# Kernel optimization log

Measured on AMD Instinct MI355X. Metric: run time of the kernel, lower is better.

Reference implementation:

```python
import jax, jax.numpy as jnp
import numpy as np
import math

EMBED_DIM = 256
NUM_HEADS = 8
FFN_DIM = 1024
EPS = 1e-5


def layer_norm(x, g, b):
    mu = jnp.mean(x, axis=-1, keepdims=True)
    var = jnp.var(x, axis=-1, keepdims=True)
    return (x - mu) / jnp.sqrt(var + EPS) * g + b


def setup_inputs() -> dict:
    key = jax.random.key(0)
    ks = jax.random.split(key, 10)
    B, L, D, F = 4, 2048, EMBED_DIM, FFN_DIM
    x = jax.random.normal(ks[0], (B, L, D), dtype=jnp.float32)
    mask = jnp.ones((B, L), dtype=jnp.int32)
    # FFN params (PyTorch Linear default-ish scale)
    W1 = jax.random.normal(ks[1], (D, F), dtype=jnp.float32) / np.sqrt(D)
    b1 = jnp.zeros((F,), dtype=jnp.float32)
    W2 = jax.random.normal(ks[2], (F, D), dtype=jnp.float32) / np.sqrt(F)
    b2 = jnp.zeros((D,), dtype=jnp.float32)
    g1 = jnp.ones((D,), dtype=jnp.float32)
    be1 = jnp.zeros((D,), dtype=jnp.float32)
    g2 = jnp.ones((D,), dtype=jnp.float32)
    be2 = jnp.zeros((D,), dtype=jnp.float32)
    return {"x": x, "mask": mask, "W1": W1, "b1": b1, "W2": W2, "b2": b2,
            "g1": g1, "be1": be1, "g2": g2, "be2": be2}


def quantum_attention(x, mask):
    B, L, D = x.shape
    H, dk = NUM_HEADS, D // NUM_HEADS
    xh = x.reshape(B, L, H, dk).transpose(0, 2, 1, 3)  # [B,H,L,dk]
    # per-token mean over batch and heads -> [L, dk]
    m = jnp.mean(xh, axis=(0, 1))
    # closed form of the single-qubit RX circuit: P(|1>) = sin^2(angle/2)
    dot = m @ m.T  # [L, L]
    ang = jnp.clip(dot, -math.pi, math.pi)
    scores = jnp.sin(ang * 0.5) ** 2  # [L, L], shared across B and H
    attn = jnp.broadcast_to(scores[None, None], (B, H, L, L))
    attn = jnp.where(mask[:, None, None, :] == 0, -1e9, attn)
    attn = jax.nn.softmax(attn, axis=-1)
    out = jnp.einsum('bhij,bhjd->bhid', attn, xh)  # values are xh itself
    return out.transpose(0, 2, 1, 3).reshape(B, L, D)


def reference(x, mask, W1, b1, W2, b2, g1, be1, g2, be2):
    attn_out = quantum_attention(x, mask)
    h = layer_norm(x + attn_out, g1, be1)
    ffn = jax.nn.relu(h @ W1 + b1) @ W2 + b2
    return layer_norm(h + ffn, g2, be2)
```

## Files before the change

kernel.cpp:

```cpp
#include <hip/hip_runtime.h>
#include <hip/hip_bf16.h>


#define B_ 4
#define L_ 2048
#define D_ 256
#define F_ 1024
#define PI_F 3.14159265358979323846f

typedef __bf16 bf16x8 __attribute__((ext_vector_type(8)));
typedef float floatx4 __attribute__((ext_vector_type(4)));
typedef unsigned short ushortx4 __attribute__((ext_vector_type(4)));
typedef unsigned short ushortx8 __attribute__((ext_vector_type(8)));

#define WAIT_VM(n) asm volatile("s_waitcnt vmcnt(" #n ")" ::: "memory")
#define WAIT_LGKM() asm volatile("s_waitcnt lgkmcnt(0)" ::: "memory")
#define SCHED0() __builtin_amdgcn_sched_barrier(0)
#define BARRIER() do { SCHED0(); __builtin_amdgcn_s_barrier(); SCHED0(); } while (0)

__device__ __forceinline__ unsigned short f2bf(float f) {
    unsigned int u = __float_as_uint(f);
    u = (u + 0x7FFFu + ((u >> 16) & 1u)) >> 16;
    return (unsigned short)u;
}
__device__ __forceinline__ float bf2f(unsigned short u) {
    union { unsigned int i; float f; } v; v.i = ((unsigned int)u) << 16; return v.f;
}

__device__ __forceinline__ void async_cp16(unsigned short* lds, const unsigned short* g) {
    __builtin_amdgcn_global_load_lds(
        (const __attribute__((address_space(1))) unsigned int*)g,
        (__attribute__((address_space(3))) unsigned int*)lds, 16, 0, 0);
}

__global__ __launch_bounds__(256) void k_prep(const float* __restrict__ x,
                                              const float* __restrict__ W1,
                                              const float* __restrict__ W2,
                                              const int* __restrict__ mask,
                                              unsigned short* __restrict__ mb,
                                              unsigned short* __restrict__ XmT,
                                              unsigned short* __restrict__ W1T,
                                              unsigned short* __restrict__ W2T) {
    __shared__ float tile[32][33];
    int r = blockIdx.x, t = threadIdx.x;
    if (r >= 2560) {
        if (r < 2816) {
            int idx = (r - 2560) * 256 + t;
            int l = idx >> 5, k = idx & 31;
            float s = 0.f;
#pragma unroll
            for (int b = 0; b < B_; b++) {
                const float* xp = x + ((size_t)(b * L_ + l)) * D_ + k;
#pragma unroll
                for (int h = 0; h < 8; h++) s += xp[h * 32];
            }
            mb[idx] = f2bf(s * (1.f / 32.f));
        } else {
#pragma unroll
            for (int c = 0; c < 32; c++) {
                int e = c * 256 + t;
                int b = e >> 11, j = e & (L_ - 1);
                XmT[(size_t)(1024 + b) * L_ + j] = mask[b * L_ + j] ? 0x3F80 : 0;
            }
        }
        return;
    }
    const float* in; unsigned short* outp; int R, C; const int* mrow = nullptr; size_t bo = 0;
    int bx, by;
    if (r < 2048) {
        int z = r >> 9, rem = r & 511; by = rem >> 3; bx = rem & 7;
        in = x; outp = XmT; R = L_; C = 256; bo = (size_t)z * R * C; mrow = mask + z * L_;
    } else if (r < 2304) {
        int rem = r - 2048; bx = rem & 31; by = rem >> 5;
        in = W1; outp = W1T; R = 256; C = 1024;
    } else {
        int rem = r - 2304; bx = rem & 7; by = rem >> 3;
        in = W2; outp = W2T; R = 1024; C = 256;
    }
    int r0 = by * 32, c0 = bx * 32;
    int tx = t & 31, ty = t >> 5;
#pragma unroll
    for (int rr = 0; rr < 4; rr++) {
        int rw = ty + rr * 8;
        tile[rw][tx] = in[bo + (size_t)(r0 + rw) * C + c0 + tx];
    }
    float mfac = 1.f;
    if (mrow) mfac = mrow[r0 + tx] ? 1.f : 0.f;
    __syncthreads();
#pragma unroll
    for (int rr = 0; rr < 4; rr++) {
        int c = ty + rr * 8;
        outp[bo + (size_t)(c0 + c) * R + r0 + tx] = f2bf(tile[tx][c] * mfac);
    }
}

__global__ __launch_bounds__(256) void k_scores_mfma(const unsigned short* __restrict__ mb,
                                                     unsigned short* __restrict__ E) {
    const int t = threadIdx.x, lane = t & 63, wid = t >> 6;
    const int wm = (wid >> 1) * 64, wn = (wid & 1) * 32;
    const int lr = lane & 15, lq = lane >> 4;
    int m0 = blockIdx.y * 128, n0 = blockIdx.x * 64;
    bf16x8 af[4], bfr[2];
#pragma unroll
    for (int i = 0; i < 4; i++)
        af[i] = *(const bf16x8*)(mb + (size_t)(m0 + wm + i * 16 + lr) * 32 + lq * 8);
#pragma unroll
    for (int j = 0; j < 2; j++)
        bfr[j] = *(const bf16x8*)(mb + (size_t)(n0 + wn + j * 16 + lr) * 32 + lq * 8);
    floatx4 acc[4][2];
#pragma unroll
    for (int i = 0; i < 4; i++)
#pragma unroll
        for (int j = 0; j < 2; j++) {
            acc[i][j] = (floatx4){0.f, 0.f, 0.f, 0.f};
            acc[i][j] = __builtin_amdgcn_mfma_f32_16x16x32_bf16(af[i], bfr[j], acc[i][j], 0, 0, 0);
        }
#pragma unroll
    for (int i = 0; i < 4; i++)
#pragma unroll
        for (int j = 0; j < 2; j++)
#pragma unroll
            for (int r = 0; r < 4; r++) {
                int row = m0 + wm + i * 16 + lq * 4 + r;
                int col = n0 + wn + j * 16 + lr;
                float d = fminf(fmaxf(acc[i][j][r], -PI_F), PI_F);
                float sn = __sinf(0.5f * d);
                E[(size_t)row * L_ + col] = f2bf(__expf(sn * sn));
            }
}

__global__ __launch_bounds__(256) void k_av(const unsigned short* __restrict__ E,
                                            const unsigned short* __restrict__ XmT,
                                            unsigned short* __restrict__ Cb) {
    __shared__ __align__(16) unsigned short sbuf[3][128 * 64 + 64 * 64];
    const int t = threadIdx.x, lane = t & 63, wid = t >> 6;
    const int wm = (wid >> 1) * 64, wn = (wid & 1) * 32;
    const int lr = lane & 15, lq = lane >> 4;
    const int lrow = lane >> 3, lseg = lane & 7;

    int bid = blockIdx.x;
    int swz = (bid & 7) * 34 + (bid >> 3);
    int m0 = (swz / 17) * 128, n0 = (swz % 17) * 64;

    const unsigned short* Ag[4]; int sAoff[4];
#pragma unroll
    for (int q = 0; q < 4; q++) {
        int rl = wid * 32 + q * 8 + lrow;
        Ag[q] = E + (size_t)(m0 + rl) * L_ + ((lseg - rl) & 7) * 8;
        sAoff[q] = (wid * 32 + q * 8) * 64;
    }
    const unsigned short* Bg[2]; int sBoff[2];
#pragma unroll
    for (int q = 0; q < 2; q++) {
        int rl = wid * 16 + q * 8 + lrow;
        Bg[q] = XmT + (size_t)(n0 + rl) * L_ + ((lseg - rl) & 7) * 8;
        sBoff[q] = 8192 + (wid * 16 + q * 8) * 64;
    }
    int arot[4], aroff[4], brot[2], broff[2];
#pragma unroll
    for (int i = 0; i < 4; i++) { int ar = wm + i * 16 + lr; aroff[i] = ar * 64; arot[i] = lq + ar; }
#pragma unroll
    for (int j = 0; j < 2; j++) { int br = wn + j * 16 + lr; broff[j] = 8192 + br * 64; brot[j] = lq + br; }

    floatx4 acc[4][2];
#pragma unroll
    for (int i = 0; i < 4; i++)
#pragma unroll
        for (int j = 0; j < 2; j++) acc[i][j] = (floatx4){0.f, 0.f, 0.f, 0.f};

    auto stage = [&](unsigned short* base, int k0) {
#pragma unroll
        for (int q = 0; q < 4; q++) async_cp16(base + sAoff[q], Ag[q] + k0);
#pragma unroll
        for (int q = 0; q < 2; q++) async_cp16(base + sBoff[q], Bg[q] + k0);
    };
    auto compute = [&](const unsigned short* base) {
#pragma unroll
        for (int s = 0; s < 2; s++) {
            bf16x8 af[4], bfr[2];
#pragma unroll
            for (int i = 0; i < 4; i++)
                af[i] = *(const bf16x8*)(base + aroff[i] + ((s * 4 + arot[i]) & 7) * 8);
#pragma unroll
            for (int j = 0; j < 2; j++)
                bfr[j] = *(const bf16x8*)(base + broff[j] + ((s * 4 + brot[j]) & 7) * 8);
#pragma unroll
            for (int i = 0; i < 4; i++)
#pragma unroll
                for (int j = 0; j < 2; j++)
                    acc[i][j] = __builtin_amdgcn_mfma_f32_16x16x32_bf16(af[i], bfr[j], acc[i][j], 0, 0, 0);
        }
    };

    unsigned short *p0 = sbuf[0], *p1 = sbuf[1], *p2 = sbuf[2];
    stage(p0, 0); stage(p1, 64); stage(p2, 128);
    WAIT_VM(12); BARRIER();
    for (int p = 0; p < 29; ++p) {
        compute(p0);
        BARRIER();
        stage(p0, (p + 3) << 6);
        WAIT_VM(12); BARRIER();
        unsigned short* tmp = p0; p0 = p1; p1 = p2; p2 = tmp;
    }
    compute(p0);
    BARRIER();
    WAIT_VM(6); BARRIER();
    compute(p1);
    BARRIER();
    WAIT_VM(0); BARRIER();
    compute(p2);

#pragma unroll
    for (int i = 0; i < 4; i++)
#pragma unroll
        for (int j = 0; j < 2; j++)
#pragma unroll
            for (int r = 0; r < 4; r++) {
                int row = m0 + wm + i * 16 + lq * 4 + r;
                int col = n0 + wn + j * 16 + lr;
                Cb[(size_t)row * 1088 + col] = f2bf(acc[i][j][r]);
            }
}

__global__ __launch_bounds__(256, 1) void k_ffn(const float* __restrict__ x,
                                                const unsigned short* __restrict__ Cb,
                                                const unsigned short* __restrict__ W1T,
                                                const unsigned short* __restrict__ W2T,
                                                const float* __restrict__ b1,
                                                const float* __restrict__ b2,
                                                const float* __restrict__ g1, const float* __restrict__ be1,
                                                const float* __restrict__ g2, const float* __restrict__ be2,
                                                float* __restrict__ out) {
    __shared__ __align__(16) unsigned short hA[4 * 32 * 64];
    __shared__ __align__(16) unsigned short W1b[2][4 * 64 * 64];
    __shared__ __align__(16) unsigned short W2b[2][4 * 64 * 64];
    __shared__ __align__(16) unsigned short t1c[32 * 72];
    __shared__ float b1s[1024];
    __shared__ float red[4][32][2];

    const int t = threadIdx.x, lane = t & 63, wid = t >> 6;
    const int lr = lane & 15, lq = lane >> 4;
    const int half = lane >> 5, l32 = lane & 31;
    const int m0 = blockIdx.x * 32;
    const int lrow8 = lane >> 3, kk = lane & 7;

    auto stageW1 = [&](unsigned short* buf, int fc) {
#pragma unroll
        for (int q = 0; q < 8; q++) {
            int kc = q >> 1, sub = q & 1;
            int fl = sub * 32 + wid * 8 + lrow8;
            const unsigned short* src = W1T + (size_t)(fc * 64 + fl) * 256 + kc * 64 + (((kk - fl) & 7) * 8);
            async_cp16(buf + kc * 4096 + sub * 2048 + wid * 512, src);
        }
    };
    auto stageW2 = [&](unsigned short* buf, int fc) {
#pragma unroll
        for (int q = 0; q < 8; q++) {
            int nc = q >> 1, sub = q & 1;
            int nl = sub * 32 + wid * 8 + lrow8;
            const unsigned short* src = W2T + (size_t)(nc * 64 + nl) * 1024 + fc * 64 + (((kk - nl) & 7) * 8);
            async_cp16(buf + nc * 4096 + sub * 2048 + wid * 512, src);
        }
    };

    stageW1(W1b[0], 0);
    stageW2(W2b[0], 0);
    stageW1(W1b[1], 1);
    stageW2(W2b[1], 1);

#pragma unroll
    for (int q = 0; q < 4; q++) b1s[q * 256 + t] = b1[q * 256 + t];
    float4 g1a = *(const float4*)(g1 + l32 * 8);
    float4 g1b = *(const float4*)(g1 + l32 * 8 + 4);
    float4 be1a = *(const float4*)(be1 + l32 * 8);
    float4 be1b = *(const float4*)(be1 + l32 * 8 + 4);

#pragma unroll
    for (int it = 0; it < 4; it++) {
        int tloc = wid * 8 + it * 2 + half;
        int tok = m0 + tloc;
        int bi = tok >> 11, ii = tok & (L_ - 1);
        float rs = bf2f(Cb[(size_t)ii * 1088 + 1024 + bi]);
        float4 xv0 = *(const float4*)(x + (size_t)tok * D_ + l32 * 8);
        float4 xv1 = *(const float4*)(x + (size_t)tok * D_ + l32 * 8 + 4);
        ushortx8 cv = *(const ushortx8*)(Cb + (size_t)ii * 1088 + bi * 256 + l32 * 8);
        float v[8];
        v[0] = xv0.x + bf2f(cv[0]) / rs; v[1] = xv0.y + bf2f(cv[1]) / rs;
        v[2] = xv0.z + bf2f(cv[2]) / rs; v[3] = xv0.w + bf2f(cv[3]) / rs;
        v[4] = xv1.x + bf2f(cv[4]) / rs; v[5] = xv1.y + bf2f(cv[5]) / rs;
        v[6] = xv1.z + bf2f(cv[6]) / rs; v[7] = xv1.w + bf2f(cv[7]) / rs;
        float s = 0.f, s2 = 0.f;
#pragma unroll
        for (int k = 0; k < 8; k++) { s += v[k]; s2 += v[k] * v[k]; }
#pragma unroll
        for (int o = 1; o < 32; o <<= 1) { s += __shfl_xor(s, o); s2 += __shfl_xor(s2, o); }
        float mu = s * (1.f / 256.f);
        float var = s2 * (1.f / 256.f) - mu * mu;
        float rq = rsqrtf(var + 1e-5f);
        union { bf16x8 v8; unsigned short u[8]; } hv;
        hv.u[0] = f2bf((v[0] - mu) * rq * g1a.x + be1a.x);
        hv.u[1] = f2bf((v[1] - mu) * rq * g1a.y + be1a.y);
        hv.u[2] = f2bf((v[2] - mu) * rq * g1a.z + be1a.z);
        hv.u[3] = f2bf((v[3] - mu) * rq * g1a.w + be1a.w);
        hv.u[4] = f2bf((v[4] - mu) * rq * g1b.x + be1b.x);
        hv.u[5] = f2bf((v[5] - mu) * rq * g1b.y + be1b.y);
        hv.u[6] = f2bf((v[6] - mu) * rq * g1b.z + be1b.z);
        hv.u[7] = f2bf((v[7] - mu) * rq * g1b.w + be1b.w);
        *(bf16x8*)(hA + (l32 >> 3) * 2048 + tloc * 64 + ((((l32 & 7) + tloc) & 7) * 8)) = hv.v8;
    }
    WAIT_VM(0); WAIT_LGKM(); BARRIER();

    bf16x8 haf[2][8];
#pragma unroll
    for (int i = 0; i < 2; i++)
#pragma unroll
        for (int kc = 0; kc < 4; kc++)
#pragma unroll
            for (int s = 0; s < 2; s++) {
                int row = i * 16 + lr;
                haf[i][kc * 2 + s] = *(const bf16x8*)(hA + kc * 2048 + row * 64 + (((s * 4 + lq + row) & 7) * 8));
            }

    floatx4 acc[2][4];
#pragma unroll
    for (int i = 0; i < 2; i++)
#pragma unroll
        for (int j = 0; j < 4; j++) acc[i][j] = (floatx4){0.f, 0.f, 0.f, 0.f};

    const int wcol = wid * 16 + lr;

#pragma unroll 1
    for (int c = 0; c < 16; ++c) {
        unsigned short* w1cur = W1b[c & 1];
        unsigned short* w2cur = W2b[c & 1];
        WAIT_VM(24); BARRIER();

        floatx4 a1[2] = { (floatx4){0.f,0.f,0.f,0.f}, (floatx4){0.f,0.f,0.f,0.f} };
#pragma unroll
        for (int kc = 0; kc < 4; kc++)
#pragma unroll
            for (int s = 0; s < 2; s++) {
                bf16x8 bfr = *(const bf16x8*)(w1cur + kc * 4096 + wcol * 64 + (((s * 4 + lq + wcol) & 7) * 8));
                a1[0] = __builtin_amdgcn_mfma_f32_16x16x32_bf16(haf[0][kc * 2 + s], bfr, a1[0], 0, 0, 0);
                a1[1] = __builtin_amdgcn_mfma_f32_16x16x32_bf16(haf[1][kc * 2 + s], bfr, a1[1], 0, 0, 0);
            }
        BARRIER();
        stageW1(w1cur, (c + 2) & 15);

        float bv = b1s[c * 64 + wcol];
#pragma unroll
        for (int i = 0; i < 2; i++)
#pragma unroll
            for (int r = 0; r < 4; r++)
                t1c[(i * 16 + lq * 4 + r) * 72 + wcol] = f2bf(fmaxf(a1[i][r] + bv, 0.f));
        WAIT_LGKM();
        WAIT_VM(24); BARRIER();

#pragma unroll
        for (int s = 0; s < 2; s++) {
            bf16x8 af0 = *(const bf16x8*)(t1c + lr * 72 + s * 32 + lq * 8);
            bf16x8 af1 = *(const bf16x8*)(t1c + (16 + lr) * 72 + s * 32 + lq * 8);
#pragma unroll
            for (int j = 0; j < 4; j++) {
                int nl = j * 16 + lr;
                bf16x8 bfr = *(const bf16x8*)(w2cur + wid * 4096 + nl * 64 + (((s * 4 + lq + nl) & 7) * 8));
                acc[0][j] = __builtin_amdgcn_mfma_f32_16x16x32_bf16(af0, bfr, acc[0][j], 0, 0, 0);
                acc[1][j] = __builtin_amdgcn_mfma_f32_16x16x32_bf16(af1, bfr, acc[1][j], 0, 0, 0);
            }
        }
        BARRIER();
        stageW2(w2cur, (c + 2) & 15);
    }

    float psum[2][4], psq[2][4];
#pragma unroll
    for (int i = 0; i < 2; i++)
#pragma unroll
        for (int r = 0; r < 4; r++) { psum[i][r] = 0.f; psq[i][r] = 0.f; }
#pragma unroll
    for (int i = 0; i < 2; i++)
#pragma unroll
        for (int j = 0; j < 4; j++) {
            int col = wid * 64 + j * 16 + lr;
            float bv = b2[col];
            int kc = col >> 6, ks = (col >> 3) & 7, ke = col & 7;
#pragma unroll
            for (int r = 0; r < 4; r++) {
                int row = i * 16 + lq * 4 + r;
                float hres = bf2f(hA[kc * 2048 + row * 64 + (((ks + row) & 7) * 8) + ke]);
                float v = acc[i][j][r] + bv + hres;
                acc[i][j][r] = v;
                psum[i][r] += v; psq[i][r] += v * v;
            }
        }
#pragma unroll
    for (int o = 1; o < 16; o <<= 1)
#pragma unroll
        for (int i = 0; i < 2; i++)
#pragma unroll
            for (int r = 0; r < 4; r++) { psum[i][r] += __shfl_xor(psum[i][r], o); psq[i][r] += __shfl_xor(psq[i][r], o); }
    if (lr == 0) {
#pragma unroll
        for (int i = 0; i < 2; i++)
#pragma unroll
            for (int r = 0; r < 4; r++) {
                int lrow = i * 16 + lq * 4 + r;
                red[wid][lrow][0] = psum[i][r];
                red[wid][lrow][1] = psq[i][r];
            }
    }
    __syncthreads();
#pragma unroll
    for (int i = 0; i < 2; i++)
#pragma unroll
        for (int r = 0; r < 4; r++) {
            int lrow = i * 16 + lq * 4 + r;
            float s  = red[0][lrow][0] + red[1][lrow][0] + red[2][lrow][0] + red[3][lrow][0];
            float s2 = red[0][lrow][1] + red[1][lrow][1] + red[2][lrow][1] + red[3][lrow][1];
            float mu = s * (1.f / 256.f);
            float var = s2 * (1.f / 256.f) - mu * mu;
            float rc = rsqrtf(var + 1e-5f);
            int row = m0 + lrow;
#pragma unroll
            for (int j = 0; j < 4; j++) {
                int col = wid * 64 + j * 16 + lr;
                out[(size_t)row * 256 + col] = (acc[i][j][r] - mu) * rc * g2[col] + be2[col];
            }
        }
}

extern "C" void kernel_launch(void* const* d_in, const int* in_sizes, int n_in,
                              void* d_out, int out_size, void* d_ws, size_t ws_size,
                              hipStream_t stream) {
    const float* x   = (const float*)d_in[0];
    const int*  mask = (const int*)d_in[1];
    const float* W1  = (const float*)d_in[2];
    const float* b1  = (const float*)d_in[3];
    const float* W2  = (const float*)d_in[4];
    const float* b2  = (const float*)d_in[5];
    const float* g1  = (const float*)d_in[6];
    const float* be1 = (const float*)d_in[7];
    const float* g2  = (const float*)d_in[8];
    const float* be2 = (const float*)d_in[9];
    float* out = (float*)d_out;

    char* w = (char*)d_ws;
    unsigned short* mb_   = (unsigned short*)w;  w += 65536 * 2;
    unsigned short* E_    = (unsigned short*)w;  w += (size_t)L_ * L_ * 2;
    unsigned short* XmT_  = (unsigned short*)w;  w += (size_t)1088 * L_ * 2;
    unsigned short* W1T_  = (unsigned short*)w;  w += 262144 * 2;
    unsigned short* W2T_  = (unsigned short*)w;  w += 262144 * 2;
    unsigned short* Cb_   = (unsigned short*)w;  w += (size_t)L_ * 1088 * 2;

    k_prep<<<2817, 256, 0, stream>>>(x, W1, W2, mask, mb_, XmT_, W1T_, W2T_);
    k_scores_mfma<<<dim3(32, 16), 256, 0, stream>>>(mb_, E_);
    k_av<<<272, 256, 0, stream>>>(E_, XmT_, Cb_);
    k_ffn<<<256, 256, 0, stream>>>(x, Cb_, W1T_, W2T_, b1, b2, g1, be1, g2, be2, out);
}
```

Before: 137.1 us.

## Warp-specialize FFN kernel into GEMM1 and GEMM2 wave groups with software pipeline

The FFN kernel grows from 256 to 512 threads and splits them into two wave groups. One group computes the first GEMM plus ReLU into a double-buffered t1c tile, and the other runs the second GEMM one chunk behind, so both GEMMs can overlap across iterations. Each group stages only its own weight matrix, and the vmcnt waits are adjusted to match. This adds an extra pipeline stage and more waves per block, with the risk of more register pressure and heavier barrier coupling.

```diff
diff --git a/kernel.cpp b/kernel.cpp
--- a/kernel.cpp
+++ b/kernel.cpp
@@ -222,7 +222,7 @@
             }
 }
 
-__global__ __launch_bounds__(256, 1) void k_ffn(const float* __restrict__ x,
+__global__ __launch_bounds__(512, 1) void k_ffn(const float* __restrict__ x,
                                                 const unsigned short* __restrict__ Cb,
                                                 const unsigned short* __restrict__ W1T,
                                                 const unsigned short* __restrict__ W2T,
@@ -234,50 +234,50 @@
     __shared__ __align__(16) unsigned short hA[4 * 32 * 64];
     __shared__ __align__(16) unsigned short W1b[2][4 * 64 * 64];
     __shared__ __align__(16) unsigned short W2b[2][4 * 64 * 64];
-    __shared__ __align__(16) unsigned short t1c[32 * 72];
+    __shared__ __align__(16) unsigned short t1c[2][32 * 72];
     __shared__ float b1s[1024];
     __shared__ float red[4][32][2];
 
     const int t = threadIdx.x, lane = t & 63, wid = t >> 6;
+    const bool isG1 = wid < 4;
+    const int gw = wid & 3;
     const int lr = lane & 15, lq = lane >> 4;
     const int half = lane >> 5, l32 = lane & 31;
+    const int lrow8 = lane >> 3, kk = lane & 7;
     const int m0 = blockIdx.x * 32;
-    const int lrow8 = lane >> 3, kk = lane & 7;
 
     auto stageW1 = [&](unsigned short* buf, int fc) {
 #pragma unroll
         for (int q = 0; q < 8; q++) {
             int kc = q >> 1, sub = q & 1;
-            int fl = sub * 32 + wid * 8 + lrow8;
+            int fl = sub * 32 + gw * 8 + lrow8;
             const unsigned short* src = W1T + (size_t)(fc * 64 + fl) * 256 + kc * 64 + (((kk - fl) & 7) * 8);
-            async_cp16(buf + kc * 4096 + sub * 2048 + wid * 512, src);
+            async_cp16(buf + kc * 4096 + sub * 2048 + gw * 512, src);
         }
     };
     auto stageW2 = [&](unsigned short* buf, int fc) {
 #pragma unroll
         for (int q = 0; q < 8; q++) {
             int nc = q >> 1, sub = q & 1;
-            int nl = sub * 32 + wid * 8 + lrow8;
+            int nl = sub * 32 + gw * 8 + lrow8;
             const unsigned short* src = W2T + (size_t)(nc * 64 + nl) * 1024 + fc * 64 + (((kk - nl) & 7) * 8);
-            async_cp16(buf + nc * 4096 + sub * 2048 + wid * 512, src);
+            async_cp16(buf + nc * 4096 + sub * 2048 + gw * 512, src);
         }
     };
 
-    stageW1(W1b[0], 0);
-    stageW2(W2b[0], 0);
-    stageW1(W1b[1], 1);
-    stageW2(W2b[1], 1);
-
-#pragma unroll
-    for (int q = 0; q < 4; q++) b1s[q * 256 + t] = b1[q * 256 + t];
+    if (isG1) { stageW1(W1b[0], 0); stageW1(W1b[1], 1); }
+    else      { stageW2(W2b[0], 0); stageW2(W2b[1], 1); }
+
+    b1s[t] = b1[t];
+    b1s[512 + t] = b1[512 + t];
     float4 g1a = *(const float4*)(g1 + l32 * 8);
     float4 g1b = *(const float4*)(g1 + l32 * 8 + 4);
     float4 be1a = *(const float4*)(be1 + l32 * 8);
     float4 be1b = *(const float4*)(be1 + l32 * 8 + 4);
 
 #pragma unroll
-    for (int it = 0; it < 4; it++) {
-        int tloc = wid * 8 + it * 2 + half;
+    for (int it = 0; it < 2; it++) {
+        int tloc = wid * 4 + it * 2 + half;
         int tok = m0 + tloc;
         int bi = tok >> 11, ii = tok & (L_ - 1);
         float rs = bf2f(Cb[(size_t)ii * 1088 + 1024 + bi]);
@@ -311,122 +311,137 @@
     WAIT_VM(0); WAIT_LGKM(); BARRIER();
 
     bf16x8 haf[2][8];
+    if (isG1) {
+#pragma unroll
+        for (int i = 0; i < 2; i++)
+#pragma unroll
+            for (int kc = 0; kc < 4; kc++)
+#pragma unroll
+                for (int s = 0; s < 2; s++) {
+                    int row = i * 16 + lr;
+                    haf[i][kc * 2 + s] = *(const bf16x8*)(hA + kc * 2048 + row * 64 + (((s * 4 + lq + row) & 7) * 8));
+                }
+    }
+
+    floatx4 acc[2][4];
 #pragma unroll
     for (int i = 0; i < 2; i++)
 #pragma unroll
-        for (int kc = 0; kc < 4; kc++)
-#pragma unroll
-            for (int s = 0; s < 2; s++) {
-                int row = i * 16 + lr;
-                haf[i][kc * 2 + s] = *(const bf16x8*)(hA + kc * 2048 + row * 64 + (((s * 4 + lq + row) & 7) * 8));
-            }
-
-    floatx4 acc[2][4];
+        for (int j = 0; j < 4; j++) acc[i][j] = (floatx4){0.f, 0.f, 0.f, 0.f};
+
+    const int wcol = gw * 16 + lr;
+
+#pragma unroll 1
+    for (int cc = 0; cc <= 16; ++cc) {
+        if (cc >= 15) { WAIT_VM(0); } else { WAIT_VM(8); }
+        BARRIER();
+        if (isG1) {
+            if (cc < 16) {
+                const unsigned short* w1cur = W1b[cc & 1];
+                floatx4 a1[2] = { (floatx4){0.f,0.f,0.f,0.f}, (floatx4){0.f,0.f,0.f,0.f} };
+#pragma unroll
+                for (int kc = 0; kc < 4; kc++)
+#pragma unroll
+                    for (int s = 0; s < 2; s++) {
+                        bf16x8 bfr = *(const bf16x8*)(w1cur + kc * 4096 + wcol * 64 + (((s * 4 + lq + wcol) & 7) * 8));
+                        a1[0] = __builtin_amdgcn_mfma_f32_16x16x32_bf16(haf[0][kc * 2 + s], bfr, a1[0], 0, 0, 0);
+                        a1[1] = __builtin_amdgcn_mfma_f32_16x16x32_bf16(haf[1][kc * 2 + s], bfr, a1[1], 0, 0, 0);
+                    }
+                float bv = b1s[cc * 64 + wcol];
+                unsigned short* tc = t1c[cc & 1];
+#pragma unroll
+                for (int i = 0; i < 2; i++)
+#pragma unroll
+                    for (int r = 0; r < 4; r++)
+                        tc[(i * 16 + lq * 4 + r) * 72 + wcol] = f2bf(fmaxf(a1[i][r] + bv, 0.f));
+                WAIT_LGKM();
+            }
+        } else {
+            if (cc >= 1) {
+                int d = cc - 1;
+                const unsigned short* w2cur = W2b[d & 1];
+                const unsigned short* tc = t1c[d & 1];
+#pragma unroll
+                for (int s = 0; s < 2; s++) {
+                    bf16x8 af0 = *(const bf16x8*)(tc + lr * 72 + s * 32 + lq * 8);
+                    bf16x8 af1 = *(const bf16x8*)(tc + (16 + lr) * 72 + s * 32 + lq * 8);
+#pragma unroll
+                    for (int j = 0; j < 4; j++) {
+                        int nl = j * 16 + lr;
+                        bf16x8 bfr = *(const bf16x8*)(w2cur + gw * 4096 + nl * 64 + (((s * 4 + lq + nl) & 7) * 8));
+                        acc[0][j] = __builtin_amdgcn_mfma_f32_16x16x32_bf16(af0, bfr, acc[0][j], 0, 0, 0);
+                        acc[1][j] = __builtin_amdgcn_mfma_f32_16x16x32_bf16(af1, bfr, acc[1][j], 0, 0, 0);
+                    }
+                }
+            }
+        }
+        BARRIER();
+        if (isG1) {
+            if (cc <= 13) stageW1(W1b[cc & 1], cc + 2);
+        } else {
+            if (cc >= 1 && cc <= 14) stageW2(W2b[(cc - 1) & 1], cc + 1);
+        }
+    }
+
+    float psum[2][4], psq[2][4];
 #pragma unroll
     for (int i = 0; i < 2; i++)
 #pragma unroll
-        for (int j = 0; j < 4; j++) acc[i][j] = (floatx4){0.f, 0.f, 0.f, 0.f};
-
-    const int wcol = wid * 16 + lr;
-
-#pragma unroll 1
-    for (int c = 0; c < 16; ++c) {
-        unsigned short* w1cur = W1b[c & 1];
-        unsigned short* w2cur = W2b[c & 1];
-        WAIT_VM(24); BARRIER();
-
-        floatx4 a1[2] = { (floatx4){0.f,0.f,0.f,0.f}, (floatx4){0.f,0.f,0.f,0.f} };
-#pragma unroll
-        for (int kc = 0; kc < 4; kc++)
-#pragma unroll
-            for (int s = 0; s < 2; s++) {
-                bf16x8 bfr = *(const bf16x8*)(w1cur + kc * 4096 + wcol * 64 + (((s * 4 + lq + wcol) & 7) * 8));
-                a1[0] = __builtin_amdgcn_mfma_f32_16x16x32_bf16(haf[0][kc * 2 + s], bfr, a1[0], 0, 0, 0);
-                a1[1] = __builtin_amdgcn_mfma_f32_16x16x32_bf16(haf[1][kc * 2 + s], bfr, a1[1], 0, 0, 0);
-            }
-        BARRIER();
-        stageW1(w1cur, (c + 2) & 15);
-
-        float bv = b1s[c * 64 + wcol];
+        for (int r = 0; r < 4; r++) { psum[i][r] = 0.f; psq[i][r] = 0.f; }
+    if (!isG1) {
 #pragma unroll
         for (int i = 0; i < 2; i++)
 #pragma unroll
-            for (int r = 0; r < 4; r++)
-                t1c[(i * 16 + lq * 4 + r) * 72 + wcol] = f2bf(fmaxf(a1[i][r] + bv, 0.f));
-        WAIT_LGKM();
-        WAIT_VM(24); BARRIER();
-
-#pragma unroll
-        for (int s = 0; s < 2; s++) {
-            bf16x8 af0 = *(const bf16x8*)(t1c + lr * 72 + s * 32 + lq * 8);
-            bf16x8 af1 = *(const bf16x8*)(t1c + (16 + lr) * 72 + s * 32 + lq * 8);
-#pragma unroll
             for (int j = 0; j < 4; j++) {
-                int nl = j * 16 + lr;
-                bf16x8 bfr = *(const bf16x8*)(w2cur + wid * 4096 + nl * 64 + (((s * 4 + lq + nl) & 7) * 8));
-                acc[0][j] = __builtin_amdgcn_mfma_f32_16x16x32_bf16(af0, bfr, acc[0][j], 0, 0, 0);
-                acc[1][j] = __builtin_amdgcn_mfma_f32_16x16x32_bf16(af1, bfr, acc[1][j], 0, 0, 0);
-            }
-        }
-        BARRIER();
-        stageW2(w2cur, (c + 2) & 15);
-    }
-
-    float psum[2][4], psq[2][4];
-#pragma unroll
-    for (int i = 0; i < 2; i++)
-#pragma unroll
-        for (int r = 0; r < 4; r++) { psum[i][r] = 0.f; psq[i][r] = 0.f; }
-#pragma unroll
-    for (int i = 0; i < 2; i++)
-#pragma unroll
-        for (int j = 0; j < 4; j++) {
-            int col = wid * 64 + j * 16 + lr;
-            float bv = b2[col];
-            int kc = col >> 6, ks = (col >> 3) & 7, ke = col & 7;
-#pragma unroll
-            for (int r = 0; r < 4; r++) {
-                int row = i * 16 + lq * 4 + r;
-                float hres = bf2f(hA[kc * 2048 + row * 64 + (((ks + row) & 7) * 8) + ke]);
-                float v = acc[i][j][r] + bv + hres;
-                acc[i][j][r] = v;
-                psum[i][r] += v; psq[i][r] += v * v;
-            }
-        }
-#pragma unroll
-    for (int o = 1; o < 16; o <<= 1)
-#pragma unroll
-        for (int i = 0; i < 2; i++)
-#pragma unroll
-            for (int r = 0; r < 4; r++) { psum[i][r] += __shfl_xor(psum[i][r], o); psq[i][r] += __shfl_xor(psq[i][r], o); }
-    if (lr == 0) {
+                int col = gw * 64 + j * 16 + lr;
+                float bv = b2[col];
+                int kc = col >> 6, ks = (col >> 3) & 7, ke = col & 7;
+#pragma unroll
+                for (int r = 0; r < 4; r++) {
+                    int row = i * 16 + lq * 4 + r;
+                    float hres = bf2f(hA[kc * 2048 + row * 64 + (((ks + row) & 7) * 8) + ke]);
+                    float v = acc[i][j][r] + bv + hres;
+                    acc[i][j][r] = v;
+                    psum[i][r] += v; psq[i][r] += v * v;
+                }
+            }
+#pragma unroll
+        for (int o = 1; o < 16; o <<= 1)
+#pragma unroll
+            for (int i = 0; i < 2; i++)
+#pragma unroll
+                for (int r = 0; r < 4; r++) { psum[i][r] += __shfl_xor(psum[i][r], o); psq[i][r] += __shfl_xor(psq[i][r], o); }
+        if (lr == 0) {
+#pragma unroll
+            for (int i = 0; i < 2; i++)
+#pragma unroll
+                for (int r = 0; r < 4; r++) {
+                    int lrow = i * 16 + lq * 4 + r;
+                    red[gw][lrow][0] = psum[i][r];
+                    red[gw][lrow][1] = psq[i][r];
+                }
+        }
+    }
+    __syncthreads();
+    if (!isG1) {
 #pragma unroll
         for (int i = 0; i < 2; i++)
 #pragma unroll
             for (int r = 0; r < 4; r++) {
                 int lrow = i * 16 + lq * 4 + r;
-                red[wid][lrow][0] = psum[i][r];
-                red[wid][lrow][1] = psq[i][r];
-            }
-    }
-    __syncthreads();
-#pragma unroll
-    for (int i = 0; i < 2; i++)
-#pragma unroll
-        for (int r = 0; r < 4; r++) {
-            int lrow = i * 16 + lq * 4 + r;
-            float s  = red[0][lrow][0] + red[1][lrow][0] + red[2][lrow][0] + red[3][lrow][0];
-            float s2 = red[0][lrow][1] + red[1][lrow][1] + red[2][lrow][1] + red[3][lrow][1];
-            float mu = s * (1.f / 256.f);
-            float var = s2 * (1.f / 256.f) - mu * mu;
-            float rc = rsqrtf(var + 1e-5f);
-            int row = m0 + lrow;
-#pragma unroll
-            for (int j = 0; j < 4; j++) {
-                int col = wid * 64 + j * 16 + lr;
-                out[(size_t)row * 256 + col] = (acc[i][j][r] - mu) * rc * g2[col] + be2[col];
-            }
-        }
+                float s  = red[0][lrow][0] + red[1][lrow][0] + red[2][lrow][0] + red[3][lrow][0];
+                float s2 = red[0][lrow][1] + red[1][lrow][1] + red[2][lrow][1] + red[3][lrow][1];
+                float mu = s * (1.f / 256.f);
+                float var = s2 * (1.f / 256.f) - mu * mu;
+                float rc = rsqrtf(var + 1e-5f);
+                int row = m0 + lrow;
+#pragma unroll
+                for (int j = 0; j < 4; j++) {
+                    int col = gw * 64 + j * 16 + lr;
+                    out[(size_t)row * 256 + col] = (acc[i][j][r] - mu) * rc * g2[col] + be2[col];
+                }
+            }
+    }
 }
 
 extern "C" void kernel_launch(void* const* d_in, const int* in_sizes, int n_in,
@@ -455,5 +470,5 @@
     k_prep<<<2817, 256, 0, stream>>>(x, W1, W2, mask, mb_, XmT_, W1T_, W2T_);
     k_scores_mfma<<<dim3(32, 16), 256, 0, stream>>>(mb_, E_);
     k_av<<<272, 256, 0, stream>>>(E_, XmT_, Cb_);
-    k_ffn<<<256, 256, 0, stream>>>(x, Cb_, W1T_, W2T_, b1, b2, g1, be1, g2, be2, out);
-}
+    k_ffn<<<256, 512, 0, stream>>>(x, Cb_, W1T_, W2T_, b1, b2, g1, be1, g2, be2, out);
+}
```

Result: faster. 133.3 us (-2.8%).
